# Optimization experiments

Measured on AMD Instinct MI355X. Metric: run time of the kernel, lower is better.

## Reference

```python
import jax, jax.numpy as jnp
import numpy as np

B, S, D = 2, 2048, 2048
H = 1024          # per-expert swiglu hidden
E = 16            # num_experts
K = 2             # top_k
T = B * S
CAP = (K * T) // E  # capacity = top_k * tokens / experts * capacity_factor(1.0) = 512


def setup_inputs() -> dict:
    key = jax.random.key(0)
    ks = jax.random.split(key, 10)
    s = 0.02
    return {
        "hidden_states": jax.random.normal(ks[0], (B, S, D), jnp.float32),
        "gate_w": jax.random.normal(ks[1], (D, E), jnp.float32) * s,
        "w1": jax.random.normal(ks[2], (E, D, H), jnp.float32) * s,
        "w3": jax.random.normal(ks[3], (E, D, H), jnp.float32) * s,
        "w2": jax.random.normal(ks[4], (E, H, D), jnp.float32) * s,
        "sw1": jax.random.normal(ks[5], (D, H), jnp.float32) * s,
        "sw3": jax.random.normal(ks[6], (D, H), jnp.float32) * s,
        "sw2": jax.random.normal(ks[7], (H, D), jnp.float32) * s,
        "coef_w": jax.random.normal(ks[8], (D, 2), jnp.float32) * s,
        "coef_b": jnp.zeros((2,), jnp.float32),
    }


def _topk_gating(logits):
    """GShard-style top-k capacity gating. logits: [T,E] (gate runs in fp32).
    Returns combine [T,E,C], dispatch [T,E,C], l_aux scalar, exp_counts [E]."""
    probs = jax.nn.softmax(logits, axis=-1)                     # [T,E]
    top_vals, top_idx = jax.lax.top_k(probs, K)                 # [T,K]
    gates = top_vals / jnp.sum(top_vals, -1, keepdims=True)     # renormalize top-k
    masks = jax.nn.one_hot(top_idx, E, dtype=probs.dtype)       # [T,K,E]

    prior = jnp.zeros((E,), probs.dtype)
    combine = jnp.zeros((T, E, CAP), probs.dtype)
    for kk in range(K):  # fixed tiny K, structurally distinct slots
        m = masks[:, kk]                                        # [T,E]
        loc = jnp.cumsum(m, axis=0) - m + prior                 # position in expert buffer
        prior = prior + jnp.sum(m, axis=0)
        keep = m * (loc < CAP)                                  # capacity drop
        pos = jnp.sum(loc * m, axis=1).astype(jnp.int32)        # [T]
        loc_oh = jax.nn.one_hot(pos, CAP, dtype=probs.dtype)    # [T,C]
        combine = combine + gates[:, kk, None, None] * keep[:, :, None] * loc_oh[:, None, :]
    dispatch = (combine > 0).astype(probs.dtype)

    # load-balancing aux loss over top-1 assignment (GShard/DeepSpeed convention)
    me = jnp.mean(probs, axis=0)                                # [E]
    ce = jnp.mean(masks[:, 0], axis=0)                          # [E]
    l_aux = jnp.sum(me * ce) * E
    exp_counts = jnp.sum(masks, axis=(0, 1)).astype(jnp.int32)  # tokens routed per expert
    return combine, dispatch, l_aux, exp_counts


def _swiglu(x, a, b, c):
    return (jax.nn.silu(x @ a) * (x @ b)) @ c


def reference(hidden_states, gate_w, w1, w3, w2, sw1, sw3, sw2, coef_w, coef_b):
    x = hidden_states.reshape(T, D)
    logits = (x.astype(jnp.float32) @ gate_w)                   # gate kept in fp32
    combine, dispatch, l_aux, exp_counts = _topk_gating(logits)

    # dispatch -> grouped expert swiglu -> combine
    xe = jnp.einsum('tec,td->ecd', dispatch.astype(x.dtype), x)         # [E,C,D]
    h = jax.nn.silu(jnp.einsum('ecd,edh->ech', xe, w1)) * jnp.einsum('ecd,edh->ech', xe, w3)
    ye = jnp.einsum('ech,ehd->ecd', h, w2)                              # [E,C,D]
    moe_out = jnp.einsum('tec,ecd->td', combine.astype(x.dtype), ye)    # [T,D]

    # shared-expert residual MLP + softmax coefficient combine
    mlp_out = _swiglu(x, sw1, sw3, sw2)                                 # [T,D]
    coef = jax.nn.softmax(x @ coef_w + coef_b, axis=-1)                 # [T,2]
    out = moe_out * coef[:, 0:1] + mlp_out * coef[:, 1:2]
    return out.reshape(B, S, D), l_aux, exp_counts
```

## Files before the change

### kernel.cpp

```cpp
#include <hip/hip_runtime.h>
#include <hip/hip_bf16.h>
#include <stdint.h>

#define T_TOK 4096
#define DIM   2048
#define HID   1024
#define NE    16
#define CAPE  512

typedef __bf16 bf16x8 __attribute__((ext_vector_type(8)));
typedef float  f32x4  __attribute__((ext_vector_type(4)));

__device__ __forceinline__ ushort f2bf(float f) {
    union { float f; uint32_t u; } v; v.f = f;
    uint32_t r = (v.u + 0x7FFFu + ((v.u >> 16) & 1u)) >> 16;
    return (ushort)r;
}
__device__ __forceinline__ float bf2f(ushort u) {
    union { uint32_t u; float f; } v; v.u = (uint32_t)u << 16; return v.f;
}
__device__ __forceinline__ void gload16(const void* g, void* lds) {
    __builtin_amdgcn_global_load_lds(
        (const __attribute__((address_space(1))) uint32_t*)g,
        (__attribute__((address_space(3))) uint32_t*)lds, 16, 0, 0);
}
#define VMCNT(n) asm volatile("s_waitcnt vmcnt(" #n ")" ::: "memory")

__global__ __launch_bounds__(256) void logits_kernel(
    const float* __restrict__ x, const float* __restrict__ gate_w,
    const float* __restrict__ coef_w, const float* __restrict__ coef_b,
    ushort* __restrict__ xb,
    int* __restrict__ topidx, float* __restrict__ gatesw,
    float* __restrict__ coefo, float* __restrict__ probs_part,
    float* __restrict__ laux)
{
    __shared__ float gws[18 * 512];
    __shared__ float wred[4][NE];
    int tid = threadIdx.x;
    int wv = tid >> 6, lane = tid & 63;
    int tbase = blockIdx.x * 16 + wv * 4;
    float acc[4][18];
#pragma unroll
    for (int tk = 0; tk < 4; ++tk)
#pragma unroll
        for (int o = 0; o < 18; ++o) acc[tk][o] = 0.f;

    for (int c = 0; c < 4; ++c) {
        int d0 = c * 512;
        __syncthreads();
        const float4* g4 = (const float4*)(gate_w + (size_t)d0 * NE);
        for (int i = tid; i < 2048; i += 256) {
            float4 v = g4[i];
            int dd = i >> 2, o0 = (i & 3) * 4;
            gws[(o0 + 0) * 512 + dd] = v.x;
            gws[(o0 + 1) * 512 + dd] = v.y;
            gws[(o0 + 2) * 512 + dd] = v.z;
            gws[(o0 + 3) * 512 + dd] = v.w;
        }
        for (int i = tid; i < 1024; i += 256) {
            float v = coef_w[(size_t)d0 * 2 + i];
            gws[(16 + (i & 1)) * 512 + (i >> 1)] = v;
        }
        __syncthreads();
#pragma unroll
        for (int tk = 0; tk < 4; ++tk) {
            int t = tbase + tk;
            const float* xr = x + (size_t)t * DIM + d0;
            float xv[8];
#pragma unroll
            for (int j = 0; j < 8; ++j) xv[j] = xr[j * 64 + lane];
#pragma unroll
            for (int j = 0; j < 8; ++j)
                xb[(size_t)t * DIM + d0 + j * 64 + lane] = f2bf(xv[j]);
#pragma unroll
            for (int o = 0; o < 18; ++o) {
                const float* gr = &gws[o * 512 + lane];
                float a = acc[tk][o];
#pragma unroll
                for (int j = 0; j < 8; ++j) a += xv[j] * gr[j * 64];
                acc[tk][o] = a;
            }
        }
    }
#pragma unroll
    for (int tk = 0; tk < 4; ++tk)
#pragma unroll
        for (int off = 32; off > 0; off >>= 1)
#pragma unroll
            for (int o = 0; o < 18; ++o)
                acc[tk][o] += __shfl_down(acc[tk][o], off, 64);

    if (lane == 0) {
        float ps[NE];
#pragma unroll
        for (int e = 0; e < NE; ++e) ps[e] = 0.f;
#pragma unroll
        for (int tk = 0; tk < 4; ++tk) {
            int t = tbase + tk;
            float lg[18];
#pragma unroll
            for (int o = 0; o < 18; ++o) lg[o] = acc[tk][o];
            float m = lg[0];
#pragma unroll
            for (int e = 1; e < NE; ++e) m = fmaxf(m, lg[e]);
            float p[NE];
            float ssum = 0.f;
#pragma unroll
            for (int e = 0; e < NE; ++e) { p[e] = expf(lg[e] - m); ssum += p[e]; }
            float inv = 1.f / ssum;
#pragma unroll
            for (int e = 0; e < NE; ++e) p[e] *= inv;
            int i1 = 0;
#pragma unroll
            for (int e = 1; e < NE; ++e) if (p[e] > p[i1]) i1 = e;
            int i2 = -1;
#pragma unroll
            for (int e = 0; e < NE; ++e) { if (e == i1) continue; if (i2 < 0 || p[e] > p[i2]) i2 = e; }
            float g0 = p[i1], g1 = p[i2], gs = g0 + g1;
            topidx[t * 2 + 0] = i1; topidx[t * 2 + 1] = i2;
            gatesw[t * 2 + 0] = g0 / gs; gatesw[t * 2 + 1] = g1 / gs;
            float c0 = lg[16] + coef_b[0], c1 = lg[17] + coef_b[1];
            float cm = fmaxf(c0, c1);
            float e0 = expf(c0 - cm), e1 = expf(c1 - cm);
            float cs = e0 + e1;
            coefo[t * 2 + 0] = e0 / cs; coefo[t * 2 + 1] = e1 / cs;
#pragma unroll
            for (int e = 0; e < NE; ++e) ps[e] += p[e];
        }
#pragma unroll
        for (int e = 0; e < NE; ++e) wred[wv][e] = ps[e];
    }
    __syncthreads();
    if (tid < NE)
        probs_part[blockIdx.x * NE + tid] =
            wred[0][tid] + wred[1][tid] + wred[2][tid] + wred[3][tid];
    if (blockIdx.x == 0 && tid == 0) laux[0] = 0.f;
}

__global__ __launch_bounds__(256) void scan_transpose(
    const int* __restrict__ topidx, const float* __restrict__ gatesw,
    const float* __restrict__ probs_part,
    int* __restrict__ sidx, float* __restrict__ swt,
    int* __restrict__ assign_token, int* __restrict__ nvalid,
    float* __restrict__ out_tail,
    const float* __restrict__ w1, const float* __restrict__ w3,
    const float* __restrict__ w2, const float* __restrict__ sw1,
    const float* __restrict__ sw3, const float* __restrict__ sw2,
    ushort* __restrict__ w1T, ushort* __restrict__ w3T, ushort* __restrict__ w2T,
    ushort* __restrict__ sw1T, ushort* __restrict__ sw3T, ushort* __restrict__ sw2T)
{
    __shared__ __align__(16) ushort tile[128][264];
    int tid = threadIdx.x;

    if (blockIdx.x < NE) {
        __shared__ int wcnt[4];
        __shared__ float fred[4];
        __shared__ int runs;
        __shared__ int cnt0s;
        int e = blockIdx.x;
        int wv = tid >> 6, ln = tid & 63;
        unsigned long long ltmask = (1ull << ln) - 1ull;
        if (tid == 0) runs = 0;
        __syncthreads();
        for (int kk = 0; kk < 2; ++kk) {
            for (int c = 0; c < T_TOK; c += 256) {
                int t = c + tid;
                bool m = (topidx[t * 2 + kk] == e);
                unsigned long long b = __ballot(m);
                int within = __popcll(b & ltmask);
                if (ln == 0) wcnt[wv] = __popcll(b);
                __syncthreads();
                int cross = 0;
                for (int w = 0; w < wv; ++w) cross += wcnt[w];
                int pos = runs + cross + within;
                if (m) {
                    bool keep = pos < CAPE;
                    sidx[t * 2 + kk] = keep ? (e * CAPE + pos) : -1;
                    swt[t * 2 + kk] = keep ? gatesw[t * 2 + kk] : 0.f;
                    if (keep) assign_token[e * CAPE + pos] = t;
                }
                __syncthreads();
                if (tid == 0) runs += wcnt[0] + wcnt[1] + wcnt[2] + wcnt[3];
                __syncthreads();
            }
            if (kk == 0 && tid == 0) cnt0s = runs;
            __syncthreads();
        }
        for (int p = runs + tid; p < CAPE; p += 256)
            assign_token[e * CAPE + p] = 0;
        float val = probs_part[tid * NE + e];
#pragma unroll
        for (int off = 32; off > 0; off >>= 1) val += __shfl_down(val, off, 64);
        if (ln == 0) fred[wv] = val;
        __syncthreads();
        if (tid == 0) {
            float psum = fred[0] + fred[1] + fred[2] + fred[3];
            int total = runs;
            nvalid[e] = min(CAPE, total);
            out_tail[1 + e] = (float)total;
            float term = (psum / (float)T_TOK) * ((float)cnt0s / (float)T_TOK) * (float)NE;
            atomicAdd(&out_tail[0], term);
        }
        return;
    }

    int id = blockIdx.x - NE;
    const float* in; ushort* outp; int R, C, tx, ty;
    if (id < 3072) {
        int seg = id >> 10;
        int rem = id & 1023;
        int e = rem >> 6;
        int r2 = rem & 63;
        if (seg < 2) {
            R = DIM; C = HID; tx = r2 & 7; ty = r2 >> 3;
            in   = (seg ? w3 : w1) + (size_t)e * DIM * HID;
            outp = (seg ? w3T : w1T) + (size_t)e * HID * DIM;
        } else {
            R = HID; C = DIM; tx = r2 & 3; ty = r2 >> 2;
            in   = w2 + (size_t)e * HID * DIM;
            outp = w2T + (size_t)e * DIM * HID;
        }
    } else {
        int id2 = id - 3072;
        int seg = id2 >> 6;
        int r2 = id2 & 63;
        if (seg < 2) {
            R = DIM; C = HID; tx = r2 & 7; ty = r2 >> 3;
            in = seg ? sw3 : sw1; outp = seg ? sw3T : sw1T;
        } else {
            R = HID; C = DIM; tx = r2 & 3; ty = r2 >> 2;
            in = sw2; outp = sw2T;
        }
    }
    int r0 = tx * 256, c0 = ty * 128;
    int t31 = tid & 31, t8 = tid >> 5;

#pragma unroll
    for (int it = 0; it < 8; ++it) {
        int r4 = (it * 8 + t8) * 4;
        int c4 = t31 * 4;
        const float* ip = in + (size_t)(r0 + r4) * C + c0 + c4;
        float va[4][4];
        *(float4*)va[0] = *(const float4*)(ip);
        *(float4*)va[1] = *(const float4*)(ip + C);
        *(float4*)va[2] = *(const float4*)(ip + 2 * (size_t)C);
        *(float4*)va[3] = *(const float4*)(ip + 3 * (size_t)C);
#pragma unroll
        for (int j = 0; j < 4; ++j) {
            uint2 u;
            u.x = (uint32_t)f2bf(va[0][j]) | ((uint32_t)f2bf(va[1][j]) << 16);
            u.y = (uint32_t)f2bf(va[2][j]) | ((uint32_t)f2bf(va[3][j]) << 16);
            *(uint2*)&tile[c4 + j][r4] = u;
        }
    }
    __syncthreads();

#pragma unroll
    for (int it = 0; it < 16; ++it) {
        int c = it * 8 + t8;
        int k = t31 * 8;
        uint4 o = *(const uint4*)&tile[c][k];
        *(uint4*)(outp + (size_t)(c0 + c) * R + r0 + k) = o;
    }
}

__device__ __forceinline__ void stage_half_off(
    const ushort* __restrict__ G, int k0, char* region, int tid,
    size_t off0, size_t off1)
{
#pragma unroll
    for (int q = 0; q < 2; ++q) {
        int c = q * 512 + tid;
        int row = c >> 3;
        int cb = (c & 7) << 4;
        int scb = cb ^ ((row & 7) << 4);
        const ushort* src = G + (q ? off1 : off0) + k0 + (scb >> 1);
        gload16(src, region + ((c - (tid & 63)) << 4));
    }
}

__device__ __forceinline__ bf16x8 ldfrag(const char* lds, int region, int row, int cb) {
    return *(const bf16x8*)(lds + region + row * 128 + (cb ^ ((row & 7) << 4)));
}

template<int NB>
__device__ __forceinline__ void core_single(
    const ushort* __restrict__ A, const ushort* __restrict__ B,
    size_t a0, size_t a1, size_t a2, size_t a3,
    size_t b0, size_t b1, size_t b2, size_t b3,
    int K, char* lds, f32x4 (&acc)[8][NB], int tid)
{
    const int DB = 32768 + NB * 8192;
    int lane = tid & 63;
    int wid = tid >> 6;
    int wrow = wid >> 2, wcol = wid & 3;
    int l15 = lane & 15, hi = lane >> 4;

#pragma unroll
    for (int m = 0; m < 8; ++m)
#pragma unroll
        for (int n = 0; n < NB; ++n)
            acc[m][n] = (f32x4){0.f, 0.f, 0.f, 0.f};

    int nj = K >> 7;

    stage_half_off(A, 0, lds + 0,           tid, a0, a1);
    stage_half_off(A, 0, lds + 16384,       tid, a2, a3);
    stage_half_off(B, 0, lds + 32768,       tid, b0, b1);
    if (NB == 4) stage_half_off(B, 0, lds + 32768 + 16384, tid, b2, b3);
    stage_half_off(B, 64, lds + DB + 32768, tid, b0, b1);
    if (NB == 4) stage_half_off(B, 64, lds + DB + 32768 + 16384, tid, b2, b3);
    if (NB == 4) VMCNT(4); else VMCNT(2);
    __builtin_amdgcn_s_barrier();
    __builtin_amdgcn_sched_barrier(0);

    for (int j = 0; j < nj; ++j) {
        int k1 = (2 * j + 1) << 6, k2 = (2 * j + 2) << 6, k3 = (2 * j + 3) << 6;
        bool st = (j < nj - 1);
#pragma unroll
        for (int d = 0; d < 2; ++d) {
            char* LA = lds + d * DB;
            char* LB = LA + 32768;
            char* LAo = lds + (d ^ 1) * DB;
            bf16x8 bf[NB][2];
#pragma unroll
            for (int p = 0; p < 4; ++p) {
                if (p == 0) {
#pragma unroll
                    for (int n = 0; n < NB; ++n)
#pragma unroll
                        for (int ks = 0; ks < 2; ++ks)
                            bf[n][ks] = ldfrag(LB, 0, wcol * (16 * NB) + n * 16 + l15, ks * 64 + hi * 16);
                }
                bf16x8 af[2][2];
#pragma unroll
                for (int i = 0; i < 2; ++i)
#pragma unroll
                    for (int ks = 0; ks < 2; ++ks)
                        af[i][ks] = ldfrag(LA, 0, wrow * 128 + (2 * p + i) * 16 + l15, ks * 64 + hi * 16);
                if (d == 0) {
                    if (p == 0)      stage_half_off(A, k1, LAo,         tid, a0, a1);
                    else if (p == 1) stage_half_off(A, k1, LAo + 16384, tid, a2, a3);
                    else if (p == 2) { if (st) stage_half_off(B, k2, LB, tid, b0, b1); }
                    else             { if (st && NB == 4) stage_half_off(B, k2, LB + 16384, tid, b2, b3); }
                } else {
                    if (st) {
                        if (p == 0)      stage_half_off(A, k2, LAo,         tid, a0, a1);
                        else if (p == 1) stage_half_off(A, k2, LAo + 16384, tid, a2, a3);
                        else if (p == 2) stage_half_off(B, k3, LB, tid, b0, b1);
                        else             { if (NB == 4) stage_half_off(B, k3, LB + 16384, tid, b2, b3); }
                    }
                }
                __builtin_amdgcn_s_barrier();
                if (p == 3) {
                    if (d == 0) {
                        if (st) { if (NB == 4) VMCNT(4); else VMCNT(2); }
                        else    VMCNT(0);
                    } else if (st) {
                        if (NB == 4) VMCNT(4); else VMCNT(2);
                    }
                }
                asm volatile("s_waitcnt lgkmcnt(0)" ::: "memory");
                __builtin_amdgcn_sched_barrier(0);
                __builtin_amdgcn_s_setprio(1);
#pragma unroll
                for (int i = 0; i < 2; ++i)
#pragma unroll
                    for (int n = 0; n < NB; ++n)
#pragma unroll
                        for (int ks = 0; ks < 2; ++ks)
                            acc[2 * p + i][n] = __builtin_amdgcn_mfma_f32_16x16x32_bf16(
                                af[i][ks], bf[n][ks], acc[2 * p + i][n], 0, 0, 0);
                __builtin_amdgcn_s_setprio(0);
                __builtin_amdgcn_s_barrier();
                __builtin_amdgcn_sched_barrier(0);
            }
        }
    }
}

template<int NM>
__device__ __forceinline__ void core_dual(
    const ushort* __restrict__ A, const ushort* __restrict__ B1,
    const ushort* __restrict__ B3,
    size_t a0, size_t a1, size_t a2, size_t a3,
    size_t b0, size_t b1,
    int K, char* lds, f32x4 (&acc1)[8][NM], f32x4 (&acc3)[8][NM], int tid)
{
    const int DB = 32768 + NM * 16384;
    int lane = tid & 63;
    int wid = tid >> 6;
    int wrow = wid >> 2, wcol = wid & 3;
    int l15 = lane & 15, hi = lane >> 4;

#pragma unroll
    for (int m = 0; m < 8; ++m)
#pragma unroll
        for (int n = 0; n < NM; ++n) {
            acc1[m][n] = (f32x4){0.f, 0.f, 0.f, 0.f};
            acc3[m][n] = (f32x4){0.f, 0.f, 0.f, 0.f};
        }

    int nj = K >> 7;

    stage_half_off(A, 0, lds + 0,     tid, a0, a1);
    stage_half_off(A, 0, lds + 16384, tid, a2, a3);
    stage_half_off(B1, 0, lds + 32768, tid, b0, b1);
    if (NM == 2) stage_half_off(B3, 0, lds + 32768 + 16384, tid, b0, b1);
    stage_half_off(B1, 64, lds + DB + 32768, tid, b0, b1);
    if (NM == 2) stage_half_off(B3, 64, lds + DB + 32768 + 16384, tid, b0, b1);
    if (NM == 2) VMCNT(4); else VMCNT(2);
    __builtin_amdgcn_s_barrier();
    __builtin_amdgcn_sched_barrier(0);

    for (int j = 0; j < nj; ++j) {
        int k1 = (2 * j + 1) << 6, k2 = (2 * j + 2) << 6, k3 = (2 * j + 3) << 6;
        bool st = (j < nj - 1);
#pragma unroll
        for (int d = 0; d < 2; ++d) {
            char* LA = lds + d * DB;
            char* LB = LA + 32768;
            char* LAo = lds + (d ^ 1) * DB;
            bf16x8 bf1[NM][2], bf3[NM][2];
#pragma unroll
            for (int p = 0; p < 4; ++p) {
                if (p == 0) {
#pragma unroll
                    for (int n = 0; n < NM; ++n)
#pragma unroll
                        for (int ks = 0; ks < 2; ++ks) {
                            int brow = wcol * (16 * NM) + n * 16 + l15;
                            bf1[n][ks] = ldfrag(LB, 0, brow,           ks * 64 + hi * 16);
                            bf3[n][ks] = ldfrag(LB, 0, brow + NM * 64, ks * 64 + hi * 16);
                        }
                }
                bf16x8 af[2][2];
#pragma unroll
                for (int i = 0; i < 2; ++i)
#pragma unroll
                    for (int ks = 0; ks < 2; ++ks)
                        af[i][ks] = ldfrag(LA, 0, wrow * 128 + (2 * p + i) * 16 + l15, ks * 64 + hi * 16);
                if (d == 0) {
                    if (p == 0)      stage_half_off(A, k1, LAo,         tid, a0, a1);
                    else if (p == 1) stage_half_off(A, k1, LAo + 16384, tid, a2, a3);
                    else if (p == 2) { if (st) stage_half_off(B1, k2, LB, tid, b0, b1); }
                    else             { if (st && NM == 2) stage_half_off(B3, k2, LB + 16384, tid, b0, b1); }
                } else {
                    if (st) {
                        if (p == 0)      stage_half_off(A, k2, LAo,         tid, a0, a1);
                        else if (p == 1) stage_half_off(A, k2, LAo + 16384, tid, a2, a3);
                        else if (p == 2) stage_half_off(B1, k3, LB, tid, b0, b1);
                        else             { if (NM == 2) stage_half_off(B3, k3, LB + 16384, tid, b0, b1); }
                    }
                }
                __builtin_amdgcn_s_barrier();
                if (p == 3) {
                    if (d == 0) {
                        if (st) { if (NM == 2) VMCNT(4); else VMCNT(2); }
                        else    VMCNT(0);
                    } else if (st) {
                        if (NM == 2) VMCNT(4); else VMCNT(2);
                    }
                }
                asm volatile("s_waitcnt lgkmcnt(0)" ::: "memory");
                __builtin_amdgcn_sched_barrier(0);
                __builtin_amdgcn_s_setprio(1);
#pragma unroll
                for (int i = 0; i < 2; ++i)
#pragma unroll
                    for (int n = 0; n < NM; ++n)
#pragma unroll
                        for (int ks = 0; ks < 2; ++ks) {
                            acc1[2 * p + i][n] = __builtin_amdgcn_mfma_f32_16x16x32_bf16(
                                af[i][ks], bf1[n][ks], acc1[2 * p + i][n], 0, 0, 0);
                            acc3[2 * p + i][n] = __builtin_amdgcn_mfma_f32_16x16x32_bf16(
                                af[i][ks], bf3[n][ks], acc3[2 * p + i][n], 0, 0, 0);
                        }
                __builtin_amdgcn_s_setprio(0);
                __builtin_amdgcn_s_barrier();
                __builtin_amdgcn_sched_barrier(0);
            }
        }
    }
}

__global__ __launch_bounds__(512, 2) void gemm8_up(
    const ushort* __restrict__ xb,
    const ushort* __restrict__ w1T, const ushort* __restrict__ w3T,
    const ushort* __restrict__ sw1T, const ushort* __restrict__ sw3T,
    const int* __restrict__ assign_token,
    ushort* __restrict__ HH, const int* __restrict__ nvalid)
{
    __shared__ __align__(16) char lds[131072];
    int b = blockIdx.x;
    int tid = threadIdx.x;
    int rr = tid >> 3;
    int lane = tid & 63, wid = tid >> 6;
    int wrow = wid >> 2, wcol = wid & 3;

    if (b < 256) {
        int id = (b & 7) * 32 + (b >> 3);
        int e = id >> 4, rem = id & 15;
        int mt = rem >> 3, nt = rem & 7;
        int bm = mt * 256, bn = nt * 128;
        if (bm >= nvalid[e]) return;
        const int* at = assign_token + e * CAPE + bm;
        size_t a0 = (size_t)at[rr] * DIM;
        size_t a1 = (size_t)at[64 + rr] * DIM;
        size_t a2 = (size_t)at[128 + rr] * DIM;
        size_t a3 = (size_t)at[192 + rr] * DIM;
        const ushort* B1 = w1T + (size_t)e * HID * DIM;
        const ushort* B3 = w3T + (size_t)e * HID * DIM;
        size_t b0 = (size_t)(bn + rr) * DIM;
        size_t b1 = (size_t)(bn + 64 + rr) * DIM;
        f32x4 acc1[8][2], acc3[8][2];
        core_dual<2>(xb, B1, B3, a0, a1, a2, a3, b0, b1, DIM, lds, acc1, acc3, tid);
        ushort* O = HH + (size_t)e * CAPE * HID;
        int rbase = bm + wrow * 128 + (lane >> 4) * 4;
        int cbase = bn + wcol * 32 + (lane & 15);
#pragma unroll
        for (int m = 0; m < 8; ++m)
#pragma unroll
            for (int n = 0; n < 2; ++n) {
                int col = cbase + n * 16;
#pragma unroll
                for (int r = 0; r < 4; ++r) {
                    float g = acc1[m][n][r];
                    float s = g / (1.f + __expf(-g));
                    O[(size_t)(rbase + m * 16 + r) * HID + col] = f2bf(s * acc3[m][n][r]);
                }
            }
    } else {
        int b2 = b - 256;
        int id = (b2 & 7) * 32 + (b2 >> 3);
        int mt = id >> 4, nt = id & 15;
        int bm = mt * 256, bn = nt * 64;
        size_t a0 = (size_t)(bm + rr) * DIM;
        size_t a1 = (size_t)(bm + 64 + rr) * DIM;
        size_t a2 = (size_t)(bm + 128 + rr) * DIM;
        size_t a3 = (size_t)(bm + 192 + rr) * DIM;
        size_t b0 = (size_t)(bn + rr) * DIM;
        size_t b1 = (size_t)(sw3T - sw1T) + (size_t)(bn + rr) * DIM;
        f32x4 acc1[8][1], acc3[8][1];
        core_dual<1>(xb, sw1T, sw1T, a0, a1, a2, a3, b0, b1, DIM, lds, acc1, acc3, tid);
        ushort* O = HH + (size_t)NE * CAPE * HID;
        int rbase = bm + wrow * 128 + (lane >> 4) * 4;
        int col = bn + wcol * 16 + (lane & 15);
#pragma unroll
        for (int m = 0; m < 8; ++m)
#pragma unroll
            for (int r = 0; r < 4; ++r) {
                float g = acc1[m][0][r];
                float s = g / (1.f + __expf(-g));
                O[(size_t)(rbase + m * 16 + r) * HID + col] = f2bf(s * acc3[m][0][r]);
            }
    }
}

__global__ __launch_bounds__(512, 2) void gemm8_down(
    const ushort* __restrict__ HH, const ushort* __restrict__ w2T,
    const ushort* __restrict__ sw2T, ushort* __restrict__ ye,
    ushort* __restrict__ mlpb, const float* __restrict__ coefo,
    const int* __restrict__ nvalid)
{
    __shared__ __align__(16) char lds[131072];
    int b = blockIdx.x;
    int tid = threadIdx.x;
    int rr = tid >> 3;
    int lane = tid & 63, wid = tid >> 6;
    int wrow = wid >> 2, wcol = wid & 3;

    if (b < 256) {
        int id = (b & 7) * 32 + (b >> 3);
        int e = id >> 4, rem = id & 15;
        int mt = rem >> 3, nt = rem & 7;
        int bm = mt * 256, bn = nt * 256;
        if (bm >= nvalid[e]) return;
        const ushort* A = HH + (size_t)e * CAPE * HID;
        const ushort* B = w2T + (size_t)e * DIM * HID;
        ushort* Ob = ye + (size_t)e * CAPE * DIM;
        size_t a0 = (size_t)(bm + rr) * HID;
        size_t a1 = (size_t)(bm + 64 + rr) * HID;
        size_t a2 = (size_t)(bm + 128 + rr) * HID;
        size_t a3 = (size_t)(bm + 192 + rr) * HID;
        size_t b0 = (size_t)(bn + rr) * HID;
        size_t b1 = (size_t)(bn + 64 + rr) * HID;
        size_t b2 = (size_t)(bn + 128 + rr) * HID;
        size_t b3 = (size_t)(bn + 192 + rr) * HID;
        f32x4 acc[8][4];
        core_single<4>(A, B, a0, a1, a2, a3, b0, b1, b2, b3, HID, lds, acc, tid);
        int rbase = bm + wrow * 128 + (lane >> 4) * 4;
        int cbase = bn + wcol * 64 + (lane & 15);
#pragma unroll
        for (int m = 0; m < 8; ++m)
#pragma unroll
            for (int n = 0; n < 4; ++n) {
                int col = cbase + n * 16;
#pragma unroll
                for (int r = 0; r < 4; ++r)
                    Ob[(size_t)(rbase + m * 16 + r) * DIM + col] = f2bf(acc[m][n][r]);
            }
    } else {
        int b2i = b - 256;
        int id = (b2i & 7) * 32 + (b2i >> 3);
        int mt = id >> 4, nt = id & 15;
        int bm = mt * 256, bn = nt * 128;
        const ushort* A = HH + (size_t)NE * CAPE * HID;
        const ushort* B = sw2T;
        size_t a0 = (size_t)(bm + rr) * HID;
        size_t a1 = (size_t)(bm + 64 + rr) * HID;
        size_t a2 = (size_t)(bm + 128 + rr) * HID;
        size_t a3 = (size_t)(bm + 192 + rr) * HID;
        size_t b0 = (size_t)(bn + rr) * HID;
        size_t b1 = (size_t)(bn + 64 + rr) * HID;
        f32x4 acc[8][2];
        core_single<2>(A, B, a0, a1, a2, a3, b0, b1, 0, 0, HID, lds, acc, tid);
        int rbase = bm + wrow * 128 + (lane >> 4) * 4;
        int cbase = bn + wcol * 32 + (lane & 15);
#pragma unroll
        for (int m = 0; m < 8; ++m)
#pragma unroll
            for (int n = 0; n < 2; ++n) {
                int col = cbase + n * 16;
#pragma unroll
                for (int r = 0; r < 4; ++r) {
                    int row = rbase + m * 16 + r;
                    mlpb[(size_t)row * DIM + col] = f2bf(acc[m][n][r] * coefo[2 * row + 1]);
                }
            }
    }
}

__global__ __launch_bounds__(256) void combine_kernel(
    const ushort* __restrict__ ye, const ushort* __restrict__ mlpb,
    const int* __restrict__ sidx, const float* __restrict__ swt,
    const float* __restrict__ coefo, float* __restrict__ out)
{
    int idx = blockIdx.x * 256 + threadIdx.x;
    int t = idx >> 9;
    int d = (idx & 511) << 2;
    int s0 = sidx[t * 2], s1 = sidx[t * 2 + 1];
    float c0 = coefo[t * 2];
    float w0 = swt[t * 2] * c0, w1 = swt[t * 2 + 1] * c0;
    uint2 mb = *(const uint2*)(mlpb + (size_t)t * DIM + d);
    const ushort* mp = (const ushort*)&mb;
    float4 v;
    v.x = bf2f(mp[0]); v.y = bf2f(mp[1]); v.z = bf2f(mp[2]); v.w = bf2f(mp[3]);
    if (s0 >= 0) {
        uint2 y = *(const uint2*)(ye + (size_t)s0 * DIM + d);
        const ushort* yp = (const ushort*)&y;
        v.x += w0 * bf2f(yp[0]); v.y += w0 * bf2f(yp[1]);
        v.z += w0 * bf2f(yp[2]); v.w += w0 * bf2f(yp[3]);
    }
    if (s1 >= 0) {
        uint2 y = *(const uint2*)(ye + (size_t)s1 * DIM + d);
        const ushort* yp = (const ushort*)&y;
        v.x += w1 * bf2f(yp[0]); v.y += w1 * bf2f(yp[1]);
        v.z += w1 * bf2f(yp[2]); v.w += w1 * bf2f(yp[3]);
    }
    *(float4*)(out + (size_t)t * DIM + d) = v;
}

extern "C" void kernel_launch(void* const* d_in, const int* in_sizes, int n_in,
                              void* d_out, int out_size, void* d_ws, size_t ws_size,
                              hipStream_t stream)
{
    const float* x      = (const float*)d_in[0];
    const float* gate_w = (const float*)d_in[1];
    const float* w1     = (const float*)d_in[2];
    const float* w3     = (const float*)d_in[3];
    const float* w2     = (const float*)d_in[4];
    const float* sw1    = (const float*)d_in[5];
    const float* sw3    = (const float*)d_in[6];
    const float* sw2    = (const float*)d_in[7];
    const float* coef_w = (const float*)d_in[8];
    const float* coef_b = (const float*)d_in[9];
    float* out = (float*)d_out;

    char* ws = (char*)d_ws;
    size_t off = 0;
    auto alloc = [&](size_t bytes) -> void* {
        void* p = ws + off;
        off += (bytes + 255) & ~(size_t)255;
        return p;
    };
    int*    nvalid       = (int*)alloc(NE * 4);
    int*    topidx       = (int*)alloc((size_t)T_TOK * 2 * 4);
    float*  gatesw       = (float*)alloc((size_t)T_TOK * 2 * 4);
    float*  coefo        = (float*)alloc((size_t)T_TOK * 2 * 4);
    int*    sidx         = (int*)alloc((size_t)T_TOK * 2 * 4);
    float*  swt          = (float*)alloc((size_t)T_TOK * 2 * 4);
    int*    assign_token = (int*)alloc((size_t)NE * CAPE * 4);
    float*  probs_part   = (float*)alloc((size_t)256 * NE * 4);
    ushort* w1T  = (ushort*)alloc((size_t)NE * HID * DIM * 2);
    ushort* w3T  = (ushort*)alloc((size_t)NE * HID * DIM * 2);
    ushort* w2T  = (ushort*)alloc((size_t)NE * DIM * HID * 2);
    ushort* sw1T = (ushort*)alloc((size_t)HID * DIM * 2);
    ushort* sw3T = (ushort*)alloc((size_t)HID * DIM * 2);
    ushort* sw2T = (ushort*)alloc((size_t)DIM * HID * 2);
    ushort* xb   = (ushort*)alloc((size_t)T_TOK * DIM * 2);
    size_t HROWS = (size_t)NE * CAPE + T_TOK;
    ushort* HH   = (ushort*)alloc(HROWS * HID * 2);
    ushort* ye   = (ushort*)alloc((size_t)NE * CAPE * DIM * 2);
    ushort* mlpb = (ushort*)alloc((size_t)T_TOK * DIM * 2);

    float* out_tail = out + (size_t)T_TOK * DIM;

    logits_kernel<<<T_TOK / 16, 256, 0, stream>>>(
        x, gate_w, coef_w, coef_b, xb, topidx, gatesw, coefo, probs_part, out_tail);
    scan_transpose<<<NE + 3264, 256, 0, stream>>>(
        topidx, gatesw, probs_part, sidx, swt, assign_token, nvalid, out_tail,
        w1, w3, w2, sw1, sw3, sw2, w1T, w3T, w2T, sw1T, sw3T, sw2T);
    gemm8_up<<<512, 512, 0, stream>>>(xb, w1T, w3T, sw1T, sw3T, assign_token, HH, nvalid);
    gemm8_down<<<512, 512, 0, stream>>>(HH, w2T, sw2T, ye, mlpb, coefo, nvalid);
    combine_kernel<<<(T_TOK * (DIM / 4)) / 256, 256, 0, stream>>>(
        ye, mlpb, sidx, swt, coefo, out);
}
```

Measured before the change: 400.5 us.

## Fuse w2 fp32-to-bf16 transpose into expert down-projection GEMM B-tile staging

Removes the separate pre-pass that converts and transposes the per-expert w2 weights to bf16. The down GEMM now loads fp32 w2 rows into registers, converts them to bf16 and writes them transposed into swizzled LDS, prefetching the next k-tile during the MFMA loop. This saves a full write and re-read of the 64MB fp32 / 32MB bf16 w2 copy. In exchange the GEMM reads fp32 (twice the bytes) and does conversion work inside the main loop, which adds register pressure.

```diff
diff --git a/kernel.cpp b/kernel.cpp
--- a/kernel.cpp
+++ b/kernel.cpp
@@ -144,9 +144,9 @@
     int* __restrict__ assign_token, int* __restrict__ nvalid,
     float* __restrict__ out_tail,
     const float* __restrict__ w1, const float* __restrict__ w3,
-    const float* __restrict__ w2, const float* __restrict__ sw1,
-    const float* __restrict__ sw3, const float* __restrict__ sw2,
-    ushort* __restrict__ w1T, ushort* __restrict__ w3T, ushort* __restrict__ w2T,
+    const float* __restrict__ sw1, const float* __restrict__ sw3,
+    const float* __restrict__ sw2,
+    ushort* __restrict__ w1T, ushort* __restrict__ w3T,
     ushort* __restrict__ sw1T, ushort* __restrict__ sw3T, ushort* __restrict__ sw2T)
 {
     __shared__ __align__(16) ushort tile[128][264];
@@ -206,22 +206,16 @@
 
     int id = blockIdx.x - NE;
     const float* in; ushort* outp; int R, C, tx, ty;
-    if (id < 3072) {
+    if (id < 2048) {
         int seg = id >> 10;
         int rem = id & 1023;
         int e = rem >> 6;
         int r2 = rem & 63;
-        if (seg < 2) {
-            R = DIM; C = HID; tx = r2 & 7; ty = r2 >> 3;
-            in   = (seg ? w3 : w1) + (size_t)e * DIM * HID;
-            outp = (seg ? w3T : w1T) + (size_t)e * HID * DIM;
-        } else {
-            R = HID; C = DIM; tx = r2 & 3; ty = r2 >> 2;
-            in   = w2 + (size_t)e * HID * DIM;
-            outp = w2T + (size_t)e * DIM * HID;
-        }
+        R = DIM; C = HID; tx = r2 & 7; ty = r2 >> 3;
+        in   = (seg ? w3 : w1) + (size_t)e * DIM * HID;
+        outp = (seg ? w3T : w1T) + (size_t)e * HID * DIM;
     } else {
-        int id2 = id - 3072;
+        int id2 = id - 2048;
         int seg = id2 >> 6;
         int r2 = id2 & 63;
         if (seg < 2) {
@@ -558,7 +552,7 @@
 }
 
 __global__ __launch_bounds__(512, 2) void gemm8_down(
-    const ushort* __restrict__ HH, const ushort* __restrict__ w2T,
+    const ushort* __restrict__ HH, const float* __restrict__ w2f,
     const ushort* __restrict__ sw2T, ushort* __restrict__ ye,
     ushort* __restrict__ mlpb, const float* __restrict__ coefo,
     const int* __restrict__ nvalid)
@@ -577,18 +571,95 @@
         int bm = mt * 256, bn = nt * 256;
         if (bm >= nvalid[e]) return;
         const ushort* A = HH + (size_t)e * CAPE * HID;
-        const ushort* B = w2T + (size_t)e * DIM * HID;
+        const float*  W = w2f + (size_t)e * HID * DIM;
         ushort* Ob = ye + (size_t)e * CAPE * DIM;
         size_t a0 = (size_t)(bm + rr) * HID;
         size_t a1 = (size_t)(bm + 64 + rr) * HID;
         size_t a2 = (size_t)(bm + 128 + rr) * HID;
         size_t a3 = (size_t)(bm + 192 + rr) * HID;
-        size_t b0 = (size_t)(bn + rr) * HID;
-        size_t b1 = (size_t)(bn + 64 + rr) * HID;
-        size_t b2 = (size_t)(bn + 128 + rr) * HID;
-        size_t b3 = (size_t)(bn + 192 + rr) * HID;
+        int nq = tid & 63;
+        int kb = (tid >> 6) * 8;
+        int l15 = lane & 15, hi = lane >> 4;
+
         f32x4 acc[8][4];
-        core_single<4>(A, B, a0, a1, a2, a3, b0, b1, b2, b3, HID, lds, acc, tid);
+#pragma unroll
+        for (int m = 0; m < 8; ++m)
+#pragma unroll
+            for (int n = 0; n < 4; ++n)
+                acc[m][n] = (f32x4){0.f, 0.f, 0.f, 0.f};
+
+        float4 breg[8];
+        stage_half_off(A, 0, lds + 0,     tid, a0, a1);
+        stage_half_off(A, 0, lds + 16384, tid, a2, a3);
+        {
+            const float* src = W + (size_t)kb * DIM + bn + nq * 4;
+#pragma unroll
+            for (int kk = 0; kk < 8; ++kk)
+                breg[kk] = *(const float4*)(src + (size_t)kk * DIM);
+        }
+        {
+            char* LB = lds + 32768;
+#pragma unroll
+            for (int j = 0; j < 4; ++j) {
+                int r = nq * 4 + j;
+                ushort pk[8];
+#pragma unroll
+                for (int kk = 0; kk < 8; ++kk) pk[kk] = f2bf(((const float*)&breg[kk])[j]);
+                int cb = (kb * 2) ^ ((r & 7) << 4);
+                *(uint4*)(LB + r * 128 + cb) = *(uint4*)pk;
+            }
+        }
+        VMCNT(0);
+        __syncthreads();
+
+        int d = 0;
+        for (int t = 0; t < HID / 64; ++t) {
+            bool pf = (t < HID / 64 - 1);
+            char* LA = lds + d * 65536;
+            char* LB = LA + 32768;
+            char* LAo = lds + (d ^ 1) * 65536;
+            char* LBo = LAo + 32768;
+            if (pf) {
+                int k0 = (t + 1) * 64;
+                stage_half_off(A, k0, LAo,         tid, a0, a1);
+                stage_half_off(A, k0, LAo + 16384, tid, a2, a3);
+                const float* src = W + (size_t)(k0 + kb) * DIM + bn + nq * 4;
+#pragma unroll
+                for (int kk = 0; kk < 8; ++kk)
+                    breg[kk] = *(const float4*)(src + (size_t)kk * DIM);
+            }
+#pragma unroll
+            for (int ks = 0; ks < 2; ++ks) {
+                bf16x8 af[8], bf[4];
+#pragma unroll
+                for (int m = 0; m < 8; ++m)
+                    af[m] = ldfrag(LA, 0, wrow * 128 + m * 16 + l15, ks * 64 + hi * 16);
+#pragma unroll
+                for (int n = 0; n < 4; ++n)
+                    bf[n] = ldfrag(LB, 0, wcol * 64 + n * 16 + l15, ks * 64 + hi * 16);
+#pragma unroll
+                for (int m = 0; m < 8; ++m)
+#pragma unroll
+                    for (int n = 0; n < 4; ++n)
+                        acc[m][n] = __builtin_amdgcn_mfma_f32_16x16x32_bf16(
+                            af[m], bf[n], acc[m][n], 0, 0, 0);
+            }
+            if (pf) {
+#pragma unroll
+                for (int j = 0; j < 4; ++j) {
+                    int r = nq * 4 + j;
+                    ushort pk[8];
+#pragma unroll
+                    for (int kk = 0; kk < 8; ++kk) pk[kk] = f2bf(((const float*)&breg[kk])[j]);
+                    int cb = (kb * 2) ^ ((r & 7) << 4);
+                    *(uint4*)(LBo + r * 128 + cb) = *(uint4*)pk;
+                }
+            }
+            VMCNT(0);
+            __syncthreads();
+            d ^= 1;
+        }
+
         int rbase = bm + wrow * 128 + (lane >> 4) * 4;
         int cbase = bn + wcol * 64 + (lane & 15);
 #pragma unroll
@@ -694,7 +765,6 @@
     float*  probs_part   = (float*)alloc((size_t)256 * NE * 4);
     ushort* w1T  = (ushort*)alloc((size_t)NE * HID * DIM * 2);
     ushort* w3T  = (ushort*)alloc((size_t)NE * HID * DIM * 2);
-    ushort* w2T  = (ushort*)alloc((size_t)NE * DIM * HID * 2);
     ushort* sw1T = (ushort*)alloc((size_t)HID * DIM * 2);
     ushort* sw3T = (ushort*)alloc((size_t)HID * DIM * 2);
     ushort* sw2T = (ushort*)alloc((size_t)DIM * HID * 2);
@@ -708,11 +778,11 @@
 
     logits_kernel<<<T_TOK / 16, 256, 0, stream>>>(
         x, gate_w, coef_w, coef_b, xb, topidx, gatesw, coefo, probs_part, out_tail);
-    scan_transpose<<<NE + 3264, 256, 0, stream>>>(
+    scan_transpose<<<NE + 2240, 256, 0, stream>>>(
         topidx, gatesw, probs_part, sidx, swt, assign_token, nvalid, out_tail,
-        w1, w3, w2, sw1, sw3, sw2, w1T, w3T, w2T, sw1T, sw3T, sw2T);
+        w1, w3, sw1, sw3, sw2, w1T, w3T, sw1T, sw3T, sw2T);
     gemm8_up<<<512, 512, 0, stream>>>(xb, w1T, w3T, sw1T, sw3T, assign_token, HH, nvalid);
-    gemm8_down<<<512, 512, 0, stream>>>(HH, w2T, sw2T, ye, mlpb, coefo, nvalid);
+    gemm8_down<<<512, 512, 0, stream>>>(HH, w2, sw2T, ye, mlpb, coefo, nvalid);
     combine_kernel<<<(T_TOK * (DIM / 4)) / 256, 256, 0, stream>>>(
         ye, mlpb, sidx, swt, coefo, out);
 }
```

After: 390.9 us. -2.4%, faster.
